# Optimization experiments

Hardware: AMD Instinct MI355X
Metric: run time of the kernel (lower is better)

Reference implementation:

```python
import jax, jax.numpy as jnp
import numpy as np


def _interp1d(xq, yq, xnew):
    """torchinterp1d semantics: linear interp with end-slope extrapolation.
    xq: (Q,) nondecreasing knots, yq: (Q,) values, xnew: any shape."""
    ind = jnp.clip(jnp.searchsorted(xq, xnew), 1, xq.shape[0] - 1)
    x0 = xq[ind - 1]
    x1 = xq[ind]
    y0 = yq[ind - 1]
    y1 = yq[ind]
    return y0 + (y1 - y0) / (x1 - x0) * (xnew - x0)


def setup_inputs() -> dict:
    key = jax.random.key(0)
    k1, k2 = jax.random.split(key)
    x = jax.random.normal(k1, (64, 512, 2048), dtype=jnp.float32)  # (N, C, L)
    target_quantiles = jax.random.uniform(k2, (256,), dtype=jnp.float32)  # sorted inside reference, as in the module
    return {"x": x, "target_quantiles": target_quantiles}


def reference(x, target_quantiles):
    # BatchOT forward (training=True, batchwise_matching=True, smoothing=None).
    C = x.shape[1]
    xt = jnp.moveaxis(x, 1, -1)        # (N, ..., C)
    flat = xt.reshape(-1, C)           # (M, C)
    Q = target_quantiles.shape[0]
    qs = jnp.linspace(0.0, 1.0, Q, dtype=x.dtype)      # buffer `quantiles`
    # per-feature batch quantiles, torch.quantile default 'linear' interpolation
    sq = jnp.quantile(flat, qs, axis=0)                # (Q, C)
    sq = jnp.sort(sq, axis=0)
    tq = jnp.sort(target_quantiles)
    # 1) map data through inverse source quantile fn, per feature: (M, C) -> [0,1]
    u = jax.vmap(_interp1d, in_axes=(1, None, 1), out_axes=1)(sq, qs, flat)
    u = jnp.clip(u, 0.0, 1.0)
    # 2) map quantile levels through the target quantile function (shared knots)
    y = _interp1d(qs, tq, u)           # (M, C)
    y = y.reshape(xt.shape)
    return jnp.moveaxis(y, -1, 1)      # (N, C, ...)
```

## Files before the change

### kernel.cpp

```cpp
#include <hip/hip_runtime.h>
#include <stdint.h>

#define N_   64
#define C_   512
#define L_   2048
#define M_   131072
#define Q_   256
#define NR_  512
#define NL_  (C_ * L_)
#define CAP_ 7168

__device__ __forceinline__ uint32_t f2u(float f) {
    uint32_t u = __float_as_uint(f);
    return u ^ ((uint32_t)((int32_t)u >> 31) | 0x80000000u);
}
__device__ __forceinline__ float u2f(uint32_t u) {
    uint32_t v = (u & 0x80000000u) ? (u ^ 0x80000000u) : ~u;
    return __uint_as_float(v);
}
__device__ __forceinline__ uint32_t h0pad(uint32_t b) { return b + (b >> 5); }

__global__ void sort_tq_kernel(const float* __restrict__ tq_in, float* __restrict__ tq_out) {
    __shared__ float s[Q_];
    int t = threadIdx.x;
    s[t] = tq_in[t];
    __syncthreads();
    for (int k = 2; k <= Q_; k <<= 1) {
        for (int j = k >> 1; j > 0; j >>= 1) {
            int ixj = t ^ j;
            if (ixj > t) {
                float a = s[t], b = s[ixj];
                bool up = ((t & k) == 0);
                if ((a > b) == up) { s[t] = b; s[ixj] = a; }
            }
            __syncthreads();
        }
    }
    tq_out[t] = s[t];
}

__device__ __forceinline__ uint32_t waveScan(uint32_t v, int lane) {
    #pragma unroll
    for (int off = 1; off < 64; off <<= 1) {
        uint32_t t = __shfl_up(v, off, 64);
        if (lane >= off) v += t;
    }
    return v;
}
__device__ __forceinline__ uint32_t blockScan(uint32_t v, uint32_t* wsum, int tid) {
    const int lane = tid & 63, wid = tid >> 6;
    uint32_t s = waveScan(v, lane);
    if (lane == 63) wsum[wid] = s;
    __syncthreads();
    if (wid == 0) {
        uint32_t w = (lane < 16) ? wsum[lane] : 0u;
        w = waveScan(w, lane);
        if (lane < 16) wsum[lane] = w;
    }
    __syncthreads();
    uint32_t r = s + ((wid > 0) ? wsum[wid - 1] : 0u);
    __syncthreads();
    return r;
}

__device__ __forceinline__ uint32_t dedupe512(uint32_t* keys, uint32_t* wsum, uint32_t* gout,
                                              uint32_t mykey, int tid, uint32_t* headOut) {
    if (tid < NR_) keys[tid] = mykey;
    __syncthreads();
    uint32_t h = 0;
    if (tid < NR_) h = (tid == 0) ? 1u : ((keys[tid] != keys[tid - 1]) ? 1u : 0u);
    uint32_t incl = blockScan(h, wsum, tid);
    if (tid == NR_ - 1) *gout = incl;
    *headOut = h;
    return incl - 1u;
}

__device__ __forceinline__ uint32_t rank_walk8(const uint32_t* rows, uint32_t slot, uint32_t& lrnk) {
    uint32_t acc = 0, dig = 0;
    bool found = false;
    const uint32_t* r = rows + slot * 17u;
    #pragma unroll
    for (int w = 0; w < 16; ++w) {
        uint32_t word = r[w];
        #pragma unroll
        for (int b = 0; b < 4; ++b) {
            uint32_t cnt = (word >> (8 * b)) & 255u;
            if (!found) {
                if (acc + cnt > lrnk) { dig = 4u * w + b; found = true; } else acc += cnt;
            }
        }
    }
    lrnk -= acc;
    return dig;
}

#define SM_KEYS 16896
#define SM_WSUM 17408
#define SM_M1   17424
#define SM_BS1  18448
#define SM_CNT2 18960
#define SM_BASE 19472
#define SM_GC   19984
#define SM_WORDS 19988

__global__ __launch_bounds__(1024, 8) void qsel_kernel(const float* __restrict__ x,
                                                       const float* __restrict__ tqs,
                                                       float* __restrict__ out) {
    __shared__ uint32_t smem[SM_WORDS];
    uint32_t* hist0    = smem;
    uint16_t* binslot  = (uint16_t*)smem;
    uint32_t* rows     = smem + 8192;
    uint32_t* candS    = smem + 8192;
    float*    ssq      = (float*)(smem + 1024);
    float4*   kt       = (float4*)(smem + 1280);
    uint32_t* tblw     = smem + 2304;
    uint16_t* tbl16    = (uint16_t*)(smem + 2304);
    uint32_t* keys     = smem + SM_KEYS;
    uint32_t* wsum     = smem + SM_WSUM;
    uint2*    m1       = (uint2*)(smem + SM_M1);
    uint32_t* bs1      = smem + SM_BS1;
    uint32_t* cnt2     = smem + SM_CNT2;
    uint32_t* base     = smem + SM_BASE;
    uint32_t* gc       = smem + SM_GC;

    const int c = blockIdx.x, tid = threadIdx.x;
    const float* xc = x + (size_t)c * L_;
    float*       oc = out + (size_t)c * L_;
    const int l4 = (tid & 511) << 2;
    const int n0 = tid >> 9;

    uint32_t lrnk = 0;
    if (tid < NR_) {
        int k = tid >> 1;
        float pos = ((float)k / 255.0f) * 131071.0f;
        int lo = (int)floorf(pos);
        if (lo > M_ - 1) lo = M_ - 1;
        if (lo < 0) lo = 0;
        int r = (tid & 1) ? ((lo + 1 > M_ - 1) ? M_ - 1 : lo + 1) : lo;
        lrnk = (uint32_t)r;
    }

    for (int i = tid; i < 16896; i += 1024) hist0[i] = 0u;
    if (tid < 4) gc[tid] = 0u;
    __syncthreads();
    for (int nn = n0; nn < N_; nn += 8) {
        float4 a = *reinterpret_cast<const float4*>(xc + (size_t)nn       * NL_ + l4);
        float4 b = *reinterpret_cast<const float4*>(xc + (size_t)(nn + 2) * NL_ + l4);
        float4 d = *reinterpret_cast<const float4*>(xc + (size_t)(nn + 4) * NL_ + l4);
        float4 e = *reinterpret_cast<const float4*>(xc + (size_t)(nn + 6) * NL_ + l4);
        float vv[16] = {a.x,a.y,a.z,a.w, b.x,b.y,b.z,b.w, d.x,d.y,d.z,d.w, e.x,e.y,e.z,e.w};
        #pragma unroll
        for (int q = 0; q < 16; ++q)
            atomicAdd(&hist0[h0pad(f2u(vv[q]) >> 18)], 1u);
    }
    __syncthreads();

    {
        uint32_t bb = (uint32_t)tid * 16u; bb += (bb >> 5);
        uint32_t acc = 0;
        #pragma unroll
        for (int i = 0; i < 16; ++i) { acc += hist0[bb + i]; hist0[bb + i] = acc; }
        uint32_t excl = blockScan(acc, wsum, tid) - acc;
        #pragma unroll
        for (int i = 0; i < 16; ++i) hist0[bb + i] += excl;
    }
    __syncthreads();

    uint32_t mykey = 0;
    if (tid < NR_) {
        uint32_t d = 0;
        #pragma unroll
        for (uint32_t s = 8192; s > 0; s >>= 1)
            if (d + s <= 16384u && hist0[h0pad(d + s - 1u)] <= lrnk) d += s;
        uint32_t below = d ? hist0[h0pad(d - 1u)] : 0u;
        mykey = d;
        lrnk -= below;
    }
    __syncthreads();

    uint32_t head;
    uint32_t slot = dedupe512(keys, wsum, gc + 0, mykey, tid, &head);

    for (int i = tid; i < 16896; i += 1024) smem[i] = (i < 8192) ? 0xFFFFFFFFu : 0u;
    if (tid < 512) m1[tid] = make_uint2(0u, 0u);
    __syncthreads();
    if (tid < NR_ && head) binslot[mykey] = (uint16_t)slot;
    __syncthreads();

    for (int nn = n0; nn < N_; nn += 8) {
        float4 a = *reinterpret_cast<const float4*>(xc + (size_t)nn       * NL_ + l4);
        float4 b = *reinterpret_cast<const float4*>(xc + (size_t)(nn + 2) * NL_ + l4);
        float4 d = *reinterpret_cast<const float4*>(xc + (size_t)(nn + 4) * NL_ + l4);
        float4 e = *reinterpret_cast<const float4*>(xc + (size_t)(nn + 6) * NL_ + l4);
        float vv[16] = {a.x,a.y,a.z,a.w, b.x,b.y,b.z,b.w, d.x,d.y,d.z,d.w, e.x,e.y,e.z,e.w};
        #pragma unroll
        for (int q = 0; q < 16; ++q) {
            uint32_t key = f2u(vv[q]);
            uint32_t s = binslot[key >> 18];
            if (s != 0xFFFFu) {
                uint32_t dd = (key >> 12) & 63u;
                atomicAdd(&rows[s * 17u + (dd >> 2)], 1u << ((dd & 3u) << 3));
            }
        }
    }
    __syncthreads();

    uint32_t dig = 0, cntg = 0;
    if (tid < NR_) {
        dig = rank_walk8(rows, slot, lrnk);
        mykey = (mykey << 6) | dig;
        cntg = (rows[slot * 17u + (dig >> 2)] >> ((dig & 3u) << 3)) & 255u;
    }
    uint32_t head1;
    uint32_t g1 = dedupe512(keys, wsum, gc + 1, mykey, tid, &head1);
    if (tid < NR_ && head1)
        atomicOr(&((uint32_t*)m1)[2u * slot + (dig >> 5)], 1u << (dig & 31u));
    if (tid < 512) cnt2[tid] = 0u;
    __syncthreads();
    {
        uint32_t S = gc[0];
        uint32_t pc = (tid < (int)S) ? (__popc(m1[tid].x) + __popc(m1[tid].y)) : 0u;
        uint32_t incl = blockScan(pc, wsum, tid);
        if (tid < 512) bs1[tid] = incl - pc;
    }
    {
        uint32_t cv = (tid < NR_ && head1) ? cntg : 0u;
        uint32_t incl = blockScan(cv, wsum, tid);
        if (tid < NR_ && head1) base[g1] = incl - cv;
        if (tid == NR_ - 1) gc[2] = incl;
    }
    __syncthreads();

    for (int nn = n0; nn < N_; nn += 8) {
        float4 a = *reinterpret_cast<const float4*>(xc + (size_t)nn       * NL_ + l4);
        float4 b = *reinterpret_cast<const float4*>(xc + (size_t)(nn + 2) * NL_ + l4);
        float4 d = *reinterpret_cast<const float4*>(xc + (size_t)(nn + 4) * NL_ + l4);
        float4 e = *reinterpret_cast<const float4*>(xc + (size_t)(nn + 6) * NL_ + l4);
        float vv[16] = {a.x,a.y,a.z,a.w, b.x,b.y,b.z,b.w, d.x,d.y,d.z,d.w, e.x,e.y,e.z,e.w};
        #pragma unroll
        for (int q = 0; q < 16; ++q) {
            uint32_t key = f2u(vv[q]);
            uint32_t s = binslot[key >> 18];
            if (s == 0xFFFFu) continue;
            uint2 mm = m1[s];
            uint32_t dd = (key >> 12) & 63u;
            uint32_t mw = (dd < 32u) ? mm.x : mm.y;
            uint32_t db = dd & 31u;
            if (!((mw >> db) & 1u)) continue;
            uint32_t g = bs1[s] + ((dd < 32u) ? __popc(mm.x & ((1u << db) - 1u))
                                              : __popc(mm.x) + __popc(mm.y & ((1u << db) - 1u)));
            uint32_t j = base[g] + atomicAdd(&cnt2[g], 1u);
            if (j < CAP_) candS[j] = key;
        }
    }
    __syncthreads();

    uint32_t G1 = gc[1];
    uint32_t total = gc[2]; if (total > CAP_) total = CAP_;
    uint32_t finalKey = 0;
    if (tid < NR_) {
        uint32_t b = base[g1];
        uint32_t n = ((g1 + 1u < G1) ? base[g1 + 1u] : total) - b;
        for (uint32_t i = 0; i < n; ++i) {
            uint32_t ki = candS[b + i];
            uint32_t clt = 0, ceq = 0;
            for (uint32_t j = 0; j < n; ++j) {
                uint32_t kj = candS[b + j];
                clt += (kj < ki) ? 1u : 0u;
                ceq += (kj == ki) ? 1u : 0u;
            }
            if (clt <= lrnk && lrnk < clt + ceq) { finalKey = ki; break; }
        }
    }
    __syncthreads();
    if (tid < NR_) keys[tid] = finalKey;
    __syncthreads();

    if (tid < Q_) {
        float pos = ((float)tid / 255.0f) * 131071.0f;
        float fr  = pos - floorf(pos);
        float vlo = u2f(keys[2 * tid]);
        float vhi = u2f(keys[2 * tid + 1]);
        ssq[tid] = vlo + fr * (vhi - vlo);
    }
    for (int i = tid; i < 8192; i += 1024) tblw[i] = 0u;
    __syncthreads();

    if (tid < Q_) {
        if (tid >= 1) {
            float x0 = ssq[tid - 1], x1 = ssq[tid];
            float y0 = tqs[tid - 1], y1 = tqs[tid];
            float dx = x1 - x0;
            kt[tid] = make_float4(x0, 1.0f / dx, y0, y1 - y0);
        }
        uint32_t kb = f2u(ssq[tid]) >> 18;
        atomicAdd(&tblw[kb >> 1], 1u << ((kb & 1u) << 4));
    }
    __syncthreads();

    {
        uint32_t bw = (uint32_t)tid * 8u;
        uint32_t w[8];
        #pragma unroll
        for (int i = 0; i < 8; ++i) w[i] = tblw[bw + i];
        uint32_t sum = 0;
        #pragma unroll
        for (int i = 0; i < 8; ++i) sum += (w[i] & 0xFFFFu) + (w[i] >> 16);
        uint32_t run = blockScan(sum, wsum, tid) - sum;
        #pragma unroll
        for (int i = 0; i < 8; ++i) {
            uint32_t c0 = w[i] & 0xFFFFu, c1 = w[i] >> 16;
            uint32_t e0 = run | (c0 ? 0x8000u : 0u); run += c0;
            uint32_t e1 = run | (c1 ? 0x8000u : 0u); run += c1;
            tblw[bw + i] = e0 | (e1 << 16);
        }
    }
    __syncthreads();

    for (int nn = n0; nn < N_; nn += 4) {
        const float4 a = *reinterpret_cast<const float4*>(xc + (size_t)nn       * NL_ + l4);
        const float4 b = *reinterpret_cast<const float4*>(xc + (size_t)(nn + 2) * NL_ + l4);
        float4 oa, ob;
        #pragma unroll
        for (int h = 0; h < 8; ++h) {
            float v = (h == 0) ? a.x : (h == 1) ? a.y : (h == 2) ? a.z : (h == 3) ? a.w
                    : (h == 4) ? b.x : (h == 5) ? b.y : (h == 6) ? b.z : b.w;
            uint32_t e = tbl16[f2u(v) >> 18];
            uint32_t t = e & 0x7FFFu;
            if (e & 0x8000u) {
                while (t < 256u && ssq[t] < v) ++t;
            }
            uint32_t ind = (t < 1u) ? 1u : ((t > 255u) ? 255u : t);
            float4 k = kt[ind];
            float r = (v - k.x) * k.y;
            r = fminf(fmaxf(r, 0.0f), 1.0f);
            float y = k.z + k.w * r;
            if      (h == 0) oa.x = y; else if (h == 1) oa.y = y;
            else if (h == 2) oa.z = y; else if (h == 3) oa.w = y;
            else if (h == 4) ob.x = y; else if (h == 5) ob.y = y;
            else if (h == 6) ob.z = y; else               ob.w = y;
        }
        *reinterpret_cast<float4*>(oc + (size_t)nn       * NL_ + l4) = oa;
        *reinterpret_cast<float4*>(oc + (size_t)(nn + 2) * NL_ + l4) = ob;
    }
}

extern "C" void kernel_launch(void* const* d_in, const int* in_sizes, int n_in,
                              void* d_out, int out_size, void* d_ws, size_t ws_size,
                              hipStream_t stream) {
    const float* x     = (const float*)d_in[0];
    const float* tq_in = (const float*)d_in[1];
    float* out = (float*)d_out;

    float* tqs = (float*)d_ws;

    sort_tq_kernel<<<1, Q_, 0, stream>>>(tq_in, tqs);
    qsel_kernel<<<C_, 1024, 0, stream>>>(x, tqs, out);
}
```

Measured before the change: 271.8 us.

## Replicate LDS histograms and lookup tables to cut bank conflicts, fuse block scans

The first-pass histogram now uses packed 16-bit counters in two replicas chosen by thread parity, which spreads LDS atomic contention; the replicas are merged during the prefix scan. The final mapping pass gets duplicated lookup table, ssq and kt copies, again picked by thread parity, to reduce LDS bank conflicts. The two block scans over slot popcounts and candidate counts are merged into one scan of packed 16-bit values, and the m1 bitmask is split into separate lo/hi arrays. The costs are more shared memory traffic for initialisation and copies, and a reliance on counts staying below 16 bits.

```diff
diff --git a/kernel.cpp b/kernel.cpp
--- a/kernel.cpp
+++ b/kernel.cpp
@@ -96,7 +96,8 @@
 
 #define SM_KEYS 16896
 #define SM_WSUM 17408
-#define SM_M1   17424
+#define SM_M1LO 17424
+#define SM_M1HI 17936
 #define SM_BS1  18448
 #define SM_CNT2 18960
 #define SM_BASE 19472
@@ -107,27 +108,32 @@
                                                        const float* __restrict__ tqs,
                                                        float* __restrict__ out) {
     __shared__ uint32_t smem[SM_WORDS];
-    uint32_t* hist0    = smem;
     uint16_t* binslot  = (uint16_t*)smem;
     uint32_t* rows     = smem + 8192;
     uint32_t* candS    = smem + 8192;
-    float*    ssq      = (float*)(smem + 1024);
-    float4*   kt       = (float4*)(smem + 1280);
-    uint32_t* tblw     = smem + 2304;
-    uint16_t* tbl16    = (uint16_t*)(smem + 2304);
     uint32_t* keys     = smem + SM_KEYS;
     uint32_t* wsum     = smem + SM_WSUM;
-    uint2*    m1       = (uint2*)(smem + SM_M1);
+    uint32_t* wsumA    = smem + 18432;
+    uint32_t* wsum2    = smem + 19968;
+    uint32_t* m1lo     = smem + SM_M1LO;
+    uint32_t* m1hi     = smem + SM_M1HI;
     uint32_t* bs1      = smem + SM_BS1;
     uint32_t* cnt2     = smem + SM_CNT2;
     uint32_t* base     = smem + SM_BASE;
     uint32_t* gc       = smem + SM_GC;
+    uint32_t* tblA     = smem;
+    uint32_t* tblB     = smem + 8192;
+    float*    ssqA     = (float*)(smem + 16384);
+    float4*   ktA      = (float4*)(smem + 16640);
+    float4*   ktB      = (float4*)(smem + 17664);
+    float*    ssqB     = (float*)(smem + 18688);
 
     const int c = blockIdx.x, tid = threadIdx.x;
     const float* xc = x + (size_t)c * L_;
     float*       oc = out + (size_t)c * L_;
     const int l4 = (tid & 511) << 2;
     const int n0 = tid >> 9;
+    const uint32_t hrep = (tid & 1) ? 9216u : 0u;
 
     uint32_t lrnk = 0;
     if (tid < NR_) {
@@ -140,7 +146,7 @@
         lrnk = (uint32_t)r;
     }
 
-    for (int i = tid; i < 16896; i += 1024) hist0[i] = 0u;
+    for (int i = tid; i < 18432; i += 1024) smem[i] = 0u;
     if (tid < 4) gc[tid] = 0u;
     __syncthreads();
     for (int nn = n0; nn < N_; nn += 8) {
@@ -150,19 +156,28 @@
         float4 e = *reinterpret_cast<const float4*>(xc + (size_t)(nn + 6) * NL_ + l4);
         float vv[16] = {a.x,a.y,a.z,a.w, b.x,b.y,b.z,b.w, d.x,d.y,d.z,d.w, e.x,e.y,e.z,e.w};
         #pragma unroll
-        for (int q = 0; q < 16; ++q)
-            atomicAdd(&hist0[h0pad(f2u(vv[q]) >> 18)], 1u);
+        for (int q = 0; q < 16; ++q) {
+            uint32_t bb = f2u(vv[q]) >> 18;
+            uint32_t w = bb >> 1; w += (w >> 3);
+            atomicAdd(&smem[hrep + w], 1u << ((bb & 1u) << 4));
+        }
     }
     __syncthreads();
 
     {
-        uint32_t bb = (uint32_t)tid * 16u; bb += (bb >> 5);
+        uint32_t r0 = 9u * (uint32_t)tid;
+        uint32_t pf[16];
         uint32_t acc = 0;
         #pragma unroll
-        for (int i = 0; i < 16; ++i) { acc += hist0[bb + i]; hist0[bb + i] = acc; }
-        uint32_t excl = blockScan(acc, wsum, tid) - acc;
-        #pragma unroll
-        for (int i = 0; i < 16; ++i) hist0[bb + i] += excl;
+        for (int i = 0; i < 8; ++i) {
+            uint32_t wa = smem[r0 + i];
+            uint32_t wb = smem[9216u + r0 + i];
+            acc += (wa & 0xFFFFu) + (wb & 0xFFFFu); pf[2 * i]     = acc;
+            acc += (wa >> 16)     + (wb >> 16);     pf[2 * i + 1] = acc;
+        }
+        uint32_t excl = blockScan(acc, wsumA, tid) - acc;
+        #pragma unroll
+        for (int i = 0; i < 16; ++i) smem[h0pad((uint32_t)tid * 16u + i)] = pf[i] + excl;
     }
     __syncthreads();
 
@@ -171,8 +186,8 @@
         uint32_t d = 0;
         #pragma unroll
         for (uint32_t s = 8192; s > 0; s >>= 1)
-            if (d + s <= 16384u && hist0[h0pad(d + s - 1u)] <= lrnk) d += s;
-        uint32_t below = d ? hist0[h0pad(d - 1u)] : 0u;
+            if (d + s <= 16384u && smem[h0pad(d + s - 1u)] <= lrnk) d += s;
+        uint32_t below = d ? smem[h0pad(d - 1u)] : 0u;
         mykey = d;
         lrnk -= below;
     }
@@ -182,7 +197,7 @@
     uint32_t slot = dedupe512(keys, wsum, gc + 0, mykey, tid, &head);
 
     for (int i = tid; i < 16896; i += 1024) smem[i] = (i < 8192) ? 0xFFFFFFFFu : 0u;
-    if (tid < 512) m1[tid] = make_uint2(0u, 0u);
+    if (tid < 512) { m1lo[tid] = 0u; m1hi[tid] = 0u; }
     __syncthreads();
     if (tid < NR_ && head) binslot[mykey] = (uint16_t)slot;
     __syncthreads();
@@ -213,21 +228,20 @@
     }
     uint32_t head1;
     uint32_t g1 = dedupe512(keys, wsum, gc + 1, mykey, tid, &head1);
-    if (tid < NR_ && head1)
-        atomicOr(&((uint32_t*)m1)[2u * slot + (dig >> 5)], 1u << (dig & 31u));
+    if (tid < NR_ && head1) {
+        if (dig < 32u) atomicOr(&m1lo[slot], 1u << dig);
+        else           atomicOr(&m1hi[slot], 1u << (dig - 32u));
+    }
     if (tid < 512) cnt2[tid] = 0u;
     __syncthreads();
     {
         uint32_t S = gc[0];
-        uint32_t pc = (tid < (int)S) ? (__popc(m1[tid].x) + __popc(m1[tid].y)) : 0u;
-        uint32_t incl = blockScan(pc, wsum, tid);
-        if (tid < 512) bs1[tid] = incl - pc;
-    }
-    {
+        uint32_t pc = (tid < (int)S) ? (__popc(m1lo[tid]) + __popc(m1hi[tid])) : 0u;
         uint32_t cv = (tid < NR_ && head1) ? cntg : 0u;
-        uint32_t incl = blockScan(cv, wsum, tid);
-        if (tid < NR_ && head1) base[g1] = incl - cv;
-        if (tid == NR_ - 1) gc[2] = incl;
+        uint32_t incl = blockScan((pc << 16) | cv, wsum, tid);
+        if (tid < 512) bs1[tid] = (incl >> 16) - pc;
+        if (tid < NR_ && head1) base[g1] = (incl & 0xFFFFu) - cv;
+        if (tid == NR_ - 1) gc[2] = incl & 0xFFFFu;
     }
     __syncthreads();
 
@@ -242,13 +256,12 @@
             uint32_t key = f2u(vv[q]);
             uint32_t s = binslot[key >> 18];
             if (s == 0xFFFFu) continue;
-            uint2 mm = m1[s];
             uint32_t dd = (key >> 12) & 63u;
-            uint32_t mw = (dd < 32u) ? mm.x : mm.y;
             uint32_t db = dd & 31u;
+            uint32_t mw = (dd < 32u) ? m1lo[s] : m1hi[s];
             if (!((mw >> db) & 1u)) continue;
-            uint32_t g = bs1[s] + ((dd < 32u) ? __popc(mm.x & ((1u << db) - 1u))
-                                              : __popc(mm.x) + __popc(mm.y & ((1u << db) - 1u)));
+            uint32_t g = bs1[s] + ((dd < 32u) ? __popc(mw & ((1u << db) - 1u))
+                                              : __popc(m1lo[s]) + __popc(mw & ((1u << db) - 1u)));
             uint32_t j = base[g] + atomicAdd(&cnt2[g], 1u);
             if (j < CAP_) candS[j] = key;
         }
@@ -281,20 +294,24 @@
         float fr  = pos - floorf(pos);
         float vlo = u2f(keys[2 * tid]);
         float vhi = u2f(keys[2 * tid + 1]);
-        ssq[tid] = vlo + fr * (vhi - vlo);
-    }
-    for (int i = tid; i < 8192; i += 1024) tblw[i] = 0u;
+        float s = vlo + fr * (vhi - vlo);
+        ssqA[tid] = s;
+        ssqB[tid] = s;
+    }
+    for (int i = tid; i < 8192; i += 1024) tblA[i] = 0u;
     __syncthreads();
 
     if (tid < Q_) {
         if (tid >= 1) {
-            float x0 = ssq[tid - 1], x1 = ssq[tid];
+            float x0 = ssqA[tid - 1], x1 = ssqA[tid];
             float y0 = tqs[tid - 1], y1 = tqs[tid];
             float dx = x1 - x0;
-            kt[tid] = make_float4(x0, 1.0f / dx, y0, y1 - y0);
-        }
-        uint32_t kb = f2u(ssq[tid]) >> 18;
-        atomicAdd(&tblw[kb >> 1], 1u << ((kb & 1u) << 4));
+            float4 k = make_float4(x0, 1.0f / dx, y0, y1 - y0);
+            ktA[tid] = k;
+            ktB[tid] = k;
+        }
+        uint32_t kb = f2u(ssqA[tid]) >> 18;
+        atomicAdd(&tblA[kb >> 1], 1u << ((kb & 1u) << 4));
     }
     __syncthreads();
 
@@ -302,21 +319,26 @@
         uint32_t bw = (uint32_t)tid * 8u;
         uint32_t w[8];
         #pragma unroll
-        for (int i = 0; i < 8; ++i) w[i] = tblw[bw + i];
+        for (int i = 0; i < 8; ++i) w[i] = tblA[bw + i];
         uint32_t sum = 0;
         #pragma unroll
         for (int i = 0; i < 8; ++i) sum += (w[i] & 0xFFFFu) + (w[i] >> 16);
-        uint32_t run = blockScan(sum, wsum, tid) - sum;
+        uint32_t run = blockScan(sum, wsum2, tid) - sum;
         #pragma unroll
         for (int i = 0; i < 8; ++i) {
             uint32_t c0 = w[i] & 0xFFFFu, c1 = w[i] >> 16;
             uint32_t e0 = run | (c0 ? 0x8000u : 0u); run += c0;
             uint32_t e1 = run | (c1 ? 0x8000u : 0u); run += c1;
-            tblw[bw + i] = e0 | (e1 << 16);
-        }
-    }
-    __syncthreads();
-
+            uint32_t ow = e0 | (e1 << 16);
+            tblA[bw + i] = ow;
+            tblB[bw + i] = ow;
+        }
+    }
+    __syncthreads();
+
+    const uint16_t* myTbl = (const uint16_t*)((tid & 1) ? tblB : tblA);
+    const float*    mySsq = (tid & 1) ? ssqB : ssqA;
+    const float4*   myKt  = (tid & 1) ? ktB  : ktA;
     for (int nn = n0; nn < N_; nn += 4) {
         const float4 a = *reinterpret_cast<const float4*>(xc + (size_t)nn       * NL_ + l4);
         const float4 b = *reinterpret_cast<const float4*>(xc + (size_t)(nn + 2) * NL_ + l4);
@@ -325,13 +347,13 @@
         for (int h = 0; h < 8; ++h) {
             float v = (h == 0) ? a.x : (h == 1) ? a.y : (h == 2) ? a.z : (h == 3) ? a.w
                     : (h == 4) ? b.x : (h == 5) ? b.y : (h == 6) ? b.z : b.w;
-            uint32_t e = tbl16[f2u(v) >> 18];
+            uint32_t e = myTbl[f2u(v) >> 18];
             uint32_t t = e & 0x7FFFu;
             if (e & 0x8000u) {
-                while (t < 256u && ssq[t] < v) ++t;
+                while (t < 256u && mySsq[t] < v) ++t;
             }
             uint32_t ind = (t < 1u) ? 1u : ((t > 255u) ? 255u : t);
-            float4 k = kt[ind];
+            float4 k = myKt[ind];
             float r = (v - k.x) * k.y;
             r = fminf(fmaxf(r, 0.0f), 1.0f);
             float y = k.z + k.w * r;
```

Result: no change. 270.2 us (-0.6%).
